# Kernel optimization log

Measured on AMD Instinct MI355X. Metric: run time of the kernel, lower is better.

## Reference

```python
import jax, jax.numpy as jnp
import numpy as np
import math

H = 16        # num_heads
HD = 64       # head_dim


def get_slopes(n):
    def pow2(n):
        start = 2 ** (-2 ** (-(math.log2(n) - 3)))
        return [start * start ** i for i in range(n)]
    if math.log2(n).is_integer():
        return pow2(n)
    c = 2 ** math.floor(math.log2(n))
    return pow2(c) + get_slopes(2 * c)[0::2][: n - c]


def setup_inputs() -> dict:
    key = jax.random.key(0)
    ks = jax.random.split(key, 6)
    b, n, d = 2, 2048, 1024
    s = 1.0 / math.sqrt(d)
    return {
        "x": jax.random.normal(ks[0], (b, n, d), jnp.float32),
        "Wq": jax.random.normal(ks[1], (d, d), jnp.float32) * s,
        "Wk": jax.random.normal(ks[2], (d, d), jnp.float32) * s,
        "Wv": jax.random.normal(ks[3], (d, d), jnp.float32) * s,
        "Wo": jax.random.normal(ks[4], (d, d), jnp.float32) * s,
        "bo": jnp.zeros((d,), jnp.float32),
    }


def reference(x, Wq, Wk, Wv, Wo, bo):
    b, n, d = x.shape
    # project and split heads: [b, H, n, HD]
    def heads(w):
        return (x @ w).reshape(b, n, H, HD).transpose(0, 2, 1, 3)
    q, k, v = heads(Wq), heads(Wk), heads(Wv)

    scores = jnp.einsum("bhqd,bhkd->bhqk", q, k)  # [b,H,n,n]
    pos = jnp.arange(n)
    dist = jnp.abs(pos[None, :] - pos[:, None]).astype(scores.dtype)  # [n,n]
    slopes = jnp.asarray(get_slopes(H), dtype=scores.dtype)
    scores = scores - slopes[:, None, None] * dist  # alibi subtracted BEFORE scaling (as in source)
    causal = pos[None, :] > pos[:, None]            # upper triangle masked
    scores = jnp.where(causal, -jnp.inf, scores)
    attn = jax.nn.softmax(scores / math.sqrt(HD), axis=-1)
    ctx = jnp.einsum("bhqk,bhkd->bhqd", attn, v)
    ctx = ctx.transpose(0, 2, 1, 3).reshape(b, n, d)
    return ctx @ Wo + bo
```

## Files before the change

### kernel.cpp

```cpp
#include <hip/hip_runtime.h>
#include <hip/hip_bf16.h>
#include <stdint.h>

#define NH 16
#define HDIM 64
#define NB 2
#define NSEQ 2048
#define DM 1024
#define MROWS (NB * NSEQ)

typedef __attribute__((ext_vector_type(8))) short bf16x8;
typedef __attribute__((ext_vector_type(4))) float f32x4;

#define MFMA32(a, b, c) __builtin_amdgcn_mfma_f32_16x16x32_bf16(a, b, c, 0, 0, 0)

static __device__ __forceinline__ unsigned short f2bf(float f) {
    union { float f; unsigned u; } v;
    v.f = f;
    unsigned r = v.u + 0x7fffu + ((v.u >> 16) & 1u);
    return (unsigned short)(r >> 16);
}

static __device__ __forceinline__ unsigned pack2bf(float a, float b) {
#if __has_builtin(__builtin_amdgcn_cvt_pk_bf16_f32)
    typedef __attribute__((ext_vector_type(2))) __bf16 bf2_t;
    union { bf2_t v; unsigned u; } c;
    c.v = __builtin_amdgcn_cvt_pk_bf16_f32(a, b);
    return c.u;
#else
    return (unsigned)f2bf(a) | ((unsigned)f2bf(b) << 16);
#endif
}

static __device__ __forceinline__ float fexp2(float x) {
#if __has_builtin(__builtin_amdgcn_exp2f)
    return __builtin_amdgcn_exp2f(x);
#else
    return exp2f(x);
#endif
}

typedef __attribute__((address_space(1))) void* gas_ptr;
typedef __attribute__((address_space(3))) void* las_ptr;

static __device__ __forceinline__ void load16_lds(const void* g, void* l) {
    __builtin_amdgcn_global_load_lds((gas_ptr)(uintptr_t)g, (las_ptr)(uintptr_t)l,
                                     16, 0, 0);
}

__global__ __launch_bounds__(256) void convert_kernel(
    const float* __restrict__ x,
    const float* __restrict__ wq, const float* __restrict__ wk,
    const float* __restrict__ wv, const float* __restrict__ wo,
    unsigned short* __restrict__ xb,
    unsigned short* __restrict__ wqkvt,
    unsigned short* __restrict__ wot)
{
    __shared__ unsigned short Ts[64][66];
    int t = threadIdx.x;
    int bx = blockIdx.x;
    if (bx < 1024) {
        const float4* xs = (const float4*)x + (long)bx * 1024;
        unsigned short* xd = xb + (long)bx * 4096;
#pragma unroll
        for (int i = 0; i < 4; i++) {
            float4 v = xs[i * 256 + t];
            ushort4 o;
            o.x = f2bf(v.x); o.y = f2bf(v.y); o.z = f2bf(v.z); o.w = f2bf(v.w);
            *(ushort4*)(xd + (i * 256 + t) * 4) = o;
        }
        return;
    }
    int wi = bx - 1024;
    int wsel = wi >> 8;
    int tile = wi & 255;
    int k0 = (tile >> 4) * 64, c0 = (tile & 15) * 64;
    const float* w = (wsel == 0) ? wq : (wsel == 1) ? wk : (wsel == 2) ? wv : wo;
    int lr = t >> 6, lc = t & 63;
#pragma unroll
    for (int rr = 0; rr < 16; rr++) {
        int row = rr * 4 + lr;
        Ts[row][lc] = f2bf(w[(long)(k0 + row) * DM + c0 + lc]);
    }
    __syncthreads();
    unsigned short* dst = (wsel == 3) ? wot : (wqkvt + (long)wsel * DM * DM);
#pragma unroll
    for (int rr = 0; rr < 16; rr++) {
        int crow = rr * 4 + lr;
        dst[(long)(c0 + crow) * DM + k0 + lc] = Ts[lc][crow];
    }
}

template<int MR>
static __device__ __forceinline__ void gemm_core_db(
    const unsigned short* __restrict__ A,
    const unsigned short* __restrict__ Bt,
    int m0, int n0,
    unsigned short* __restrict__ As,
    unsigned short* __restrict__ Bs,
    f32x4 (&acc)[MR][4])
{
    constexpr int MT  = MR * 32;
    constexpr int ASZ = MT * 32;
    constexpr int BSZ = 128 * 32;
    constexpr int NA  = MT / 64;

    int t = threadIdx.x;
    int lane = t & 63;
    int wave = t >> 6;
    int l16 = lane & 15, quad = lane >> 4;
    int wm = wave >> 1, wn = wave & 1;

    const char* gA[NA];
#pragma unroll
    for (int i = 0; i < NA; i++) {
        int b = i * 256 + t;
        int row = b >> 2, g = (b & 3) ^ ((row >> 1) & 3);
        gA[i] = (const char*)(A + (long)(m0 + row) * DM) + g * 16;
    }
    const char* gB[2];
#pragma unroll
    for (int i = 0; i < 2; i++) {
        int b = i * 256 + t;
        int row = b >> 2, g = (b & 3) ^ ((row >> 1) & 3);
        gB[i] = (const char*)(Bt + (long)(n0 + row) * DM) + g * 16;
    }

    int sread = quad ^ ((l16 >> 1) & 3);
    int faOff = (wm * (MT / 2) + l16) * 32 + sread * 8;
    int fbOff = (wn * 64 + l16) * 32 + sread * 8;

#pragma unroll
    for (int i = 0; i < NA; i++)
        load16_lds(gA[i], (char*)As + i * 4096 + t * 16);
#pragma unroll
    for (int i = 0; i < 2; i++)
        load16_lds(gB[i], (char*)Bs + i * 4096 + t * 16);

    for (int kk = 0; kk < DM; kk += 32) {
        int cur = (kk >> 5) & 1;
        __syncthreads();
        if (kk + 32 < DM) {
            int nxt = cur ^ 1;
            char* abuf = (char*)(As + nxt * ASZ);
            char* bbuf = (char*)(Bs + nxt * BSZ);
#pragma unroll
            for (int i = 0; i < NA; i++)
                load16_lds(gA[i] + (kk + 32) * 2, abuf + i * 4096 + t * 16);
#pragma unroll
            for (int i = 0; i < 2; i++)
                load16_lds(gB[i] + (kk + 32) * 2, bbuf + i * 4096 + t * 16);
        }
        const unsigned short* fa = As + cur * ASZ + faOff;
        const unsigned short* fb = Bs + cur * BSZ + fbOff;
        bf16x8 af[MR], bf[4];
#pragma unroll
        for (int r = 0; r < MR; r++) af[r] = *(const bf16x8*)(fa + r * 16 * 32);
#pragma unroll
        for (int c = 0; c < 4; c++) bf[c] = *(const bf16x8*)(fb + c * 16 * 32);
#pragma unroll
        for (int r = 0; r < MR; r++)
#pragma unroll
            for (int c = 0; c < 4; c++)
                acc[r][c] = MFMA32(af[r], bf[c], acc[r][c]);
    }
}

__global__ __launch_bounds__(256) void qkv_gemm_kernel(
    const unsigned short* __restrict__ A,
    const unsigned short* __restrict__ Bt,
    unsigned short* __restrict__ Qo, unsigned short* __restrict__ Ko,
    unsigned short* __restrict__ Vt)
{
    __shared__ unsigned short As[2][128 * 32];
    __shared__ unsigned short Bs[2][128 * 32];
    __shared__ unsigned short Tw[4][16][72];

    f32x4 acc[4][4] = {};
    int m0 = blockIdx.y * 128, n0 = blockIdx.x * 128;
    gemm_core_db<4>(A, Bt, m0, n0, &As[0][0], &Bs[0][0], acc);

    int t = threadIdx.x, wave = t >> 6, lane = t & 63;
    int l16 = lane & 15, quad = lane >> 4;
    int wm = wave >> 1, wn = wave & 1;
    int rg0 = m0 + wm * 64;
    int cg0 = n0 + wn * 64;
    int z = cg0 >> 10;
    int b_ = rg0 >> 11;
    int nb0 = rg0 & (NSEQ - 1);
    int h = (cg0 & 1023) >> 6;
    long bh = (long)(b_ * NH + h);

    if (z < 2) {
        unsigned short* dst = (z == 0 ? Qo : Ko) + bh * NSEQ * HDIM;
#pragma unroll
        for (int r = 0; r < 4; r++)
#pragma unroll
            for (int reg = 0; reg < 4; reg++) {
                long rowb = (long)(nb0 + r * 16 + quad * 4 + reg) * HDIM;
#pragma unroll
                for (int c = 0; c < 4; c++)
                    dst[rowb + c * 16 + l16] = f2bf(acc[r][c][reg]);
            }
    } else {
        unsigned short* dst = Vt + bh * HDIM * NSEQ;
#pragma unroll
        for (int c = 0; c < 4; c++) {
#pragma unroll
            for (int r = 0; r < 4; r++) {
                ushort4 u;
                u.x = f2bf(acc[r][c][0]); u.y = f2bf(acc[r][c][1]);
                u.z = f2bf(acc[r][c][2]); u.w = f2bf(acc[r][c][3]);
                *(ushort4*)&Tw[wave][l16][r * 16 + quad * 4] = u;
            }
#pragma unroll
            for (int j = 0; j < 4; j++) {
                int lrow = j * 4 + quad;
                ushort4 u = *(const ushort4*)&Tw[wave][lrow][l16 * 4];
                *(ushort4*)(dst + (long)(c * 16 + lrow) * NSEQ + nb0 + l16 * 4) = u;
            }
        }
    }
}

static __device__ __forceinline__ void softmax_fixed(
    f32x4* s, bool mask, int qb, int kb, float sc2, float mrow,
    f32x4& l_vec, unsigned pbu[2][4], int l16, int quad)
{
    if (mask) {
        int fdm = qb + l16 - kb - quad * 4;
#pragma unroll
        for (int tt = 0; tt < 4; tt++)
#pragma unroll
            for (int r = 0; r < 4; r++)
                if (tt * 16 + r > fdm) s[tt][r] = -3e38f;
    }
    f32x4 e[4];
#pragma unroll
    for (int tt = 0; tt < 4; tt++)
#pragma unroll
        for (int r = 0; r < 4; r++)
            e[tt][r] = fexp2(s[tt][r] * sc2 - mrow);
#pragma unroll
    for (int r = 0; r < 4; r++)
        l_vec[r] += (e[0][r] + e[1][r]) + (e[2][r] + e[3][r]);

#pragma unroll
    for (int p = 0; p < 2; p++) {
        pbu[p][0] = pack2bf(e[2 * p][0],     e[2 * p][1]);
        pbu[p][1] = pack2bf(e[2 * p][2],     e[2 * p][3]);
        pbu[p][2] = pack2bf(e[2 * p + 1][0], e[2 * p + 1][1]);
        pbu[p][3] = pack2bf(e[2 * p + 1][2], e[2 * p + 1][3]);
    }
}

__global__ __launch_bounds__(512) void attn_kernel(
    const unsigned short* __restrict__ Q,
    const unsigned short* __restrict__ K,
    const unsigned short* __restrict__ Vt,
    unsigned short* __restrict__ ctx)
{
    __shared__ unsigned short KV[2][8192];

    int t = threadIdx.x, w = t >> 6, lane = t & 63;
    int l16 = lane & 15, quad = lane >> 4;
    int r7 = l16 & 7;
    int bh = blockIdx.x;
    int b_ = bh >> 4, h = bh & 15;
    int pr = blockIdx.y;
    int t1 = 31 - pr, t0 = pr;
    int nch = t1 + 1;
    bool isT0 = (w >= 4);
    int myTile = isT0 ? t0 : t1;
    int myNch = myTile + 1;
    int qb = myTile * 64 + (w & 3) * 16;

    const unsigned short* Kg  = K  + (long)bh * NSEQ * HDIM;
    const unsigned short* Vtg = Vt + (long)bh * HDIM * NSEQ;

    const float log2e = 1.44269504f;
    float slope = exp2f(-0.5f * (float)(h + 1));
    float sc2 = 0.125f * log2e;
    float ss2 = slope * sc2;

    const unsigned short* qp = Q + ((long)bh * NSEQ + qb + l16) * HDIM + quad * 8;
    bf16x8 aq0 = *(const bf16x8*)qp;
    bf16x8 aq1 = *(const bf16x8*)(qp + 32);

    f32x4 cinit[4];
#pragma unroll
    for (int tt = 0; tt < 4; tt++)
#pragma unroll
        for (int r = 0; r < 4; r++)
            cinit[tt][r] = slope * (float)(tt * 16 + quad * 4 + r);

    f32x4 lv = {};
    f32x4 o[4] = {};

    int row = t >> 3, sp = t & 7, sw = sp ^ (row & 7);
    const unsigned short* gk = Kg + row * HDIM + sw * 8;
    const unsigned short* gv = Vtg + (long)row * NSEQ + sw * 8;

    {
        unsigned short* buf = KV[0];
        load16_lds(gk, buf + t * 8);
        load16_lds(gv, buf + 4096 + t * 8);
    }

    for (int c = 0; c < nch; c++) {
        __syncthreads();
        if (c + 1 < nch) {
            int kb2 = (c + 1) * 64;
            unsigned short* buf = KV[(c + 1) & 1];
            load16_lds(gk + kb2 * HDIM, buf + t * 8);
            load16_lds(gv + kb2, buf + 4096 + t * 8);
        }
        if (isT0 && c >= myNch) continue;

        const unsigned short* Ks = KV[c & 1];
        const unsigned short* Vs = KV[c & 1] + 4096;
        int kb = c * 64;

        f32x4 s[4];
#pragma unroll
        for (int tt = 0; tt < 4; tt++) {
            int rr = tt * 16 + l16;
            bf16x8 k0 = *(const bf16x8*)(Ks + (rr * 8 + (quad ^ r7)) * 8);
            bf16x8 k1 = *(const bf16x8*)(Ks + (rr * 8 + ((quad + 4) ^ r7)) * 8);
            f32x4 z = MFMA32(k0, aq0, cinit[tt]);
            s[tt] = MFMA32(k1, aq1, z);
        }

        float mrow = ss2 * (float)(qb + l16 - kb);
        unsigned pb[2][4];
        softmax_fixed(s, c == myNch - 1, qb, kb, sc2, mrow, lv, pb, l16, quad);

        int q2 = quad >> 1, q1b = (quad & 1) << 3;
#pragma unroll
        for (int cb = 0; cb < 4; cb++) {
            int rd = cb * 16 + l16;
            const char* vrow = (const char*)(Vs + rd * 64);
            int x7 = rd & 7;
#pragma unroll
            for (int p = 0; p < 2; p++) {
                union { bf16x8 v; uint2 u2[2]; } a;
                int sb0 = 4 * p + q2;
                int sb1 = 4 * p + 2 + q2;
                a.u2[0] = *(const uint2*)(vrow + ((sb0 ^ x7) << 4) + q1b);
                a.u2[1] = *(const uint2*)(vrow + ((sb1 ^ x7) << 4) + q1b);
                union { unsigned u[4]; bf16x8 v; } bv;
#pragma unroll
                for (int i = 0; i < 4; i++) bv.u[i] = pb[p][i];
                o[cb] = MFMA32(a.v, bv.v, o[cb]);
            }
        }
    }

    {
        float lt = (lv[0] + lv[1]) + (lv[2] + lv[3]);
        lt += __shfl_xor(lt, 16);
        lt += __shfl_xor(lt, 32);
        float inv = 1.0f / lt;
        long base = (((long)b_ * NSEQ + (qb + l16)) * NH + h) * HDIM + quad * 4;
#pragma unroll
        for (int cb = 0; cb < 4; cb++) {
            uint2 u;
            u.x = pack2bf(o[cb][0] * inv, o[cb][1] * inv);
            u.y = pack2bf(o[cb][2] * inv, o[cb][3] * inv);
            *(uint2*)(ctx + base + cb * 16) = u;
        }
    }
}

__global__ __launch_bounds__(256) void out_gemm_kernel(
    const unsigned short* __restrict__ A,
    const unsigned short* __restrict__ Bt,
    const float* __restrict__ bias,
    float* __restrict__ out)
{
    __shared__ unsigned short As[2][64 * 32];
    __shared__ unsigned short Bs[2][128 * 32];
    f32x4 acc[2][4] = {};
    int m0 = blockIdx.y * 64, n0 = blockIdx.x * 128;
    gemm_core_db<2>(A, Bt, m0, n0, &As[0][0], &Bs[0][0], acc);

    int t = threadIdx.x, wave = t >> 6, lane = t & 63;
    int l16 = lane & 15, quad = lane >> 4;
    int wm = wave >> 1, wn = wave & 1;
    int rg0 = m0 + wm * 32, cg0 = n0 + wn * 64;
#pragma unroll
    for (int c = 0; c < 4; c++) {
        float bc = bias[cg0 + c * 16 + l16];
#pragma unroll
        for (int r = 0; r < 2; r++)
#pragma unroll
            for (int reg = 0; reg < 4; reg++)
                out[(long)(rg0 + r * 16 + quad * 4 + reg) * DM + cg0 + c * 16 + l16] =
                    acc[r][c][reg] + bc;
    }
}

extern "C" void kernel_launch(void* const* d_in, const int* in_sizes, int n_in,
                              void* d_out, int out_size, void* d_ws, size_t ws_size,
                              hipStream_t stream)
{
    const float* x  = (const float*)d_in[0];
    const float* wq = (const float*)d_in[1];
    const float* wk = (const float*)d_in[2];
    const float* wv = (const float*)d_in[3];
    const float* wo = (const float*)d_in[4];
    const float* bo = (const float*)d_in[5];

    char* ws = (char*)d_ws;
    unsigned short* xb    = (unsigned short*)(ws);
    unsigned short* wqkvt = (unsigned short*)(ws + (8L  << 20));
    unsigned short* wot   = (unsigned short*)(ws + (14L << 20));
    unsigned short* Qb    = (unsigned short*)(ws + (16L << 20));
    unsigned short* Kb    = (unsigned short*)(ws + (24L << 20));
    unsigned short* Vt    = (unsigned short*)(ws + (32L << 20));
    unsigned short* ctx   = (unsigned short*)(ws + (40L << 20));
    float* out = (float*)d_out;

    convert_kernel<<<2048, 256, 0, stream>>>(x, wq, wk, wv, wo, xb, wqkvt, wot);

    qkv_gemm_kernel<<<dim3(3 * DM / 128, MROWS / 128), 256, 0, stream>>>(
        xb, wqkvt, Qb, Kb, Vt);

    attn_kernel<<<dim3(NB * NH, 16), 512, 0, stream>>>(Qb, Kb, Vt, ctx);

    out_gemm_kernel<<<dim3(DM / 128, MROWS / 64), 256, 0, stream>>>(
        ctx, wot, bo, out);
}
```

Measured before the change: 170.1 us.

## Remap GEMM block order per XCD, tighten launch bounds, cut attention register use

Both GEMM kernels remap the linear block id so that consecutive ids, which are dealt round-robin across the 8 XCDs, land on neighbouring tiles, aiming for better L2 reuse. The GEMM launch bounds request 3 blocks per CU and the attention kernel 4 waves-per-EU. The attention kernel computes the ALiBi init vector on the fly instead of keeping 16 registers live, and reuses the score registers for the exponentials, to lower register pressure. It also raises wave priority with s_setprio around the MFMA sections. Forcing higher occupancy risks register spills.

```diff
diff --git a/kernel.cpp b/kernel.cpp
--- a/kernel.cpp
+++ b/kernel.cpp
@@ -166,7 +166,7 @@
     }
 }
 
-__global__ __launch_bounds__(256) void qkv_gemm_kernel(
+__global__ __launch_bounds__(256, 3) void qkv_gemm_kernel(
     const unsigned short* __restrict__ A,
     const unsigned short* __restrict__ Bt,
     unsigned short* __restrict__ Qo, unsigned short* __restrict__ Ko,
@@ -177,7 +177,9 @@
     __shared__ unsigned short Tw[4][16][72];
 
     f32x4 acc[4][4] = {};
-    int m0 = blockIdx.y * 128, n0 = blockIdx.x * 128;
+    int id = blockIdx.y * 24 + blockIdx.x;
+    id = (id & 7) * 96 + (id >> 3);
+    int m0 = (id / 24) * 128, n0 = (id % 24) * 128;
     gemm_core_db<4>(A, Bt, m0, n0, &As[0][0], &Bs[0][0], acc);
 
     int t = threadIdx.x, wave = t >> 6, lane = t & 63;
@@ -235,26 +237,25 @@
             for (int r = 0; r < 4; r++)
                 if (tt * 16 + r > fdm) s[tt][r] = -3e38f;
     }
-    f32x4 e[4];
 #pragma unroll
     for (int tt = 0; tt < 4; tt++)
 #pragma unroll
         for (int r = 0; r < 4; r++)
-            e[tt][r] = fexp2(s[tt][r] * sc2 - mrow);
+            s[tt][r] = fexp2(s[tt][r] * sc2 - mrow);
 #pragma unroll
     for (int r = 0; r < 4; r++)
-        l_vec[r] += (e[0][r] + e[1][r]) + (e[2][r] + e[3][r]);
+        l_vec[r] += (s[0][r] + s[1][r]) + (s[2][r] + s[3][r]);
 
 #pragma unroll
     for (int p = 0; p < 2; p++) {
-        pbu[p][0] = pack2bf(e[2 * p][0],     e[2 * p][1]);
-        pbu[p][1] = pack2bf(e[2 * p][2],     e[2 * p][3]);
-        pbu[p][2] = pack2bf(e[2 * p + 1][0], e[2 * p + 1][1]);
-        pbu[p][3] = pack2bf(e[2 * p + 1][2], e[2 * p + 1][3]);
-    }
-}
-
-__global__ __launch_bounds__(512) void attn_kernel(
+        pbu[p][0] = pack2bf(s[2 * p][0],     s[2 * p][1]);
+        pbu[p][1] = pack2bf(s[2 * p][2],     s[2 * p][3]);
+        pbu[p][2] = pack2bf(s[2 * p + 1][0], s[2 * p + 1][1]);
+        pbu[p][3] = pack2bf(s[2 * p + 1][2], s[2 * p + 1][3]);
+    }
+}
+
+__global__ __launch_bounds__(512, 4) void attn_kernel(
     const unsigned short* __restrict__ Q,
     const unsigned short* __restrict__ K,
     const unsigned short* __restrict__ Vt,
@@ -287,12 +288,11 @@
     bf16x8 aq0 = *(const bf16x8*)qp;
     bf16x8 aq1 = *(const bf16x8*)(qp + 32);
 
-    f32x4 cinit[4];
-#pragma unroll
-    for (int tt = 0; tt < 4; tt++)
-#pragma unroll
-        for (int r = 0; r < 4; r++)
-            cinit[tt][r] = slope * (float)(tt * 16 + quad * 4 + r);
+    f32x4 ci4;
+#pragma unroll
+    for (int r = 0; r < 4; r++)
+        ci4[r] = slope * (float)(quad * 4 + r);
+    float s16 = slope * 16.0f;
 
     f32x4 lv = {};
     f32x4 o[4] = {};
@@ -322,20 +322,27 @@
         int kb = c * 64;
 
         f32x4 s[4];
+        __builtin_amdgcn_s_setprio(1);
 #pragma unroll
         for (int tt = 0; tt < 4; tt++) {
             int rr = tt * 16 + l16;
             bf16x8 k0 = *(const bf16x8*)(Ks + (rr * 8 + (quad ^ r7)) * 8);
             bf16x8 k1 = *(const bf16x8*)(Ks + (rr * 8 + ((quad + 4) ^ r7)) * 8);
-            f32x4 z = MFMA32(k0, aq0, cinit[tt]);
+            f32x4 cz;
+#pragma unroll
+            for (int r = 0; r < 4; r++)
+                cz[r] = ci4[r] + (float)tt * s16;
+            f32x4 z = MFMA32(k0, aq0, cz);
             s[tt] = MFMA32(k1, aq1, z);
         }
+        __builtin_amdgcn_s_setprio(0);
 
         float mrow = ss2 * (float)(qb + l16 - kb);
         unsigned pb[2][4];
         softmax_fixed(s, c == myNch - 1, qb, kb, sc2, mrow, lv, pb, l16, quad);
 
         int q2 = quad >> 1, q1b = (quad & 1) << 3;
+        __builtin_amdgcn_s_setprio(1);
 #pragma unroll
         for (int cb = 0; cb < 4; cb++) {
             int rd = cb * 16 + l16;
@@ -354,6 +361,7 @@
                 o[cb] = MFMA32(a.v, bv.v, o[cb]);
             }
         }
+        __builtin_amdgcn_s_setprio(0);
     }
 
     {
@@ -372,7 +380,7 @@
     }
 }
 
-__global__ __launch_bounds__(256) void out_gemm_kernel(
+__global__ __launch_bounds__(256, 3) void out_gemm_kernel(
     const unsigned short* __restrict__ A,
     const unsigned short* __restrict__ Bt,
     const float* __restrict__ bias,
@@ -381,7 +389,9 @@
     __shared__ unsigned short As[2][64 * 32];
     __shared__ unsigned short Bs[2][128 * 32];
     f32x4 acc[2][4] = {};
-    int m0 = blockIdx.y * 64, n0 = blockIdx.x * 128;
+    int id = blockIdx.y * 8 + blockIdx.x;
+    id = (id & 7) * 64 + (id >> 3);
+    int m0 = (id >> 3) * 64, n0 = (id & 7) * 128;
     gemm_core_db<2>(A, Bt, m0, n0, &As[0][0], &Bs[0][0], acc);
 
     int t = threadIdx.x, wave = t >> 6, lane = t & 63;
```

Result: no change. 168.0 us (-1.3%).
